# Performance work log

Measured on AMD Instinct MI355X. Metric: run time of the kernel, lower is better.

Reference implementation:

```python
import jax, jax.numpy as jnp
import numpy as np
import math

B = 200        # graphs
NPG = 512      # nodes per graph
EPG = 8192     # edges per graph (avg degree 16)
E = B * EPG
FIN = 11
H = 128


def setup_inputs() -> dict:
    key = jax.random.key(0)
    ks = jax.random.split(key, 16)
    g = jnp.arange(E, dtype=jnp.int32) // EPG  # graph id per edge
    edge_src = g * NPG + jax.random.randint(ks[0], (E,), 0, NPG, dtype=jnp.int32)
    edge_dst = g * NPG + jax.random.randint(ks[1], (E,), 0, NPG, dtype=jnp.int32)
    x = jax.random.normal(ks[2], (B * NPG, FIN), dtype=jnp.float32)

    def w(k, shape):
        return jax.random.normal(k, shape, dtype=jnp.float32) * 0.1

    return dict(
        x=x, edge_src=edge_src, edge_dst=edge_dst,
        num_graphs=B, nodes_per_graph=NPG,
        Wrel1=w(ks[3], (H, FIN)), Wroot1=w(ks[4], (H, FIN)), b1=jnp.zeros((H,), jnp.float32), pw1=w(ks[5], (H,)),
        Wrel2=w(ks[6], (H, H)), Wroot2=w(ks[7], (H, H)), b2=jnp.zeros((H,), jnp.float32), pw2=w(ks[8], (H,)),
        Wrel3=w(ks[9], (H, H)), Wroot3=w(ks[10], (H, H)), b3=jnp.zeros((H,), jnp.float32), pw3=w(ks[11], (H,)),
        Wl1=w(ks[12], (512, 256)), bl1=jnp.zeros((512,), jnp.float32),
        Wl2=w(ks[13], (64, 512)), bl2=jnp.zeros((64,), jnp.float32),
        Wl3=w(ks[14], (1, 64)), bl3=jnp.zeros((1,), jnp.float32),
    )


def graph_conv(x, src, dst, emask, Wrel, Wroot, b):
    # PyG GraphConv (aggr='add'): lin_rel(sum_j x_j) + lin_root(x)
    msg = x[src] * emask[:, None]                    # [E, F] gather + edge mask
    agg = jax.ops.segment_sum(msg, dst, num_segments=x.shape[0])
    return agg @ Wrel.T + b + x @ Wroot.T


def topk_pool(x, src, dst, emask, w, ratio, B):
    # PyG TopKPooling: score = tanh((x . w)/||w||), keep top ceil(ratio*N) per graph
    N = x.shape[0] // B
    k = int(math.ceil(ratio * N))
    score = jnp.tanh((x @ w) / jnp.linalg.norm(w))   # [B*N]
    _, idx = jax.lax.top_k(score.reshape(B, N), k)   # local indices per graph
    perm = (idx + (jnp.arange(B, dtype=idx.dtype) * N)[:, None]).reshape(-1)  # [B*k]
    xk = x[perm] * score[perm][:, None]
    # old node id -> new node id (or -1 if dropped); reindex edges, mask invalid
    newid = jnp.full((B * N,), -1, dtype=jnp.int32).at[perm].set(jnp.arange(B * k, dtype=jnp.int32))
    ns, nd = newid[src], newid[dst]
    keep = emask * (ns >= 0) * (nd >= 0)
    return xk, jnp.maximum(ns, 0), jnp.maximum(nd, 0), keep.astype(x.dtype)


def readout(x, B):
    # cat([global_max_pool, global_mean_pool]); uniform graph sizes -> reshape
    xr = x.reshape(B, -1, x.shape[-1])
    return jnp.concatenate([xr.max(axis=1), xr.mean(axis=1)], axis=-1)


def reference(x, edge_src, edge_dst, num_graphs, nodes_per_graph,
              Wrel1, Wroot1, b1, pw1, Wrel2, Wroot2, b2, pw2,
              Wrel3, Wroot3, b3, pw3, Wl1, bl1, Wl2, bl2, Wl3, bl3):
    Bg = num_graphs
    src, dst = edge_src, edge_dst
    emask = jnp.ones(src.shape, x.dtype)
    h = jax.nn.relu(graph_conv(x, src, dst, emask, Wrel1, Wroot1, b1))
    h, src, dst, emask = topk_pool(h, src, dst, emask, pw1, 0.5, Bg)
    x1 = readout(h, Bg)
    h = jax.nn.relu(graph_conv(h, src, dst, emask, Wrel2, Wroot2, b2))
    h, src, dst, emask = topk_pool(h, src, dst, emask, pw2, 0.8, Bg)
    x2 = readout(h, Bg)
    h = jax.nn.relu(graph_conv(h, src, dst, emask, Wrel3, Wroot3, b3))
    h, src, dst, emask = topk_pool(h, src, dst, emask, pw3, 0.8, Bg)
    x3 = readout(h, Bg)
    z = x1 + x2 + x3
    z = jax.nn.relu(z @ Wl1.T + bl1)   # dropout p=0.7 is identity in eval mode
    z = jax.nn.relu(z @ Wl2.T + bl2)
    return z @ Wl3.T + bl3             # [B, 1]
```

## Files before the change

kernel.cpp:

```cpp
#include <hip/hip_runtime.h>
#include <math.h>

#define BG   200
#define NPGc 512
#define EPGc 8192
#define NE   (BG*EPGc)
#define N0   (BG*NPGc)
#define FINc 11
#define Hc   128
#define K1c  256
#define K2c  205
#define K3c  164
#define N1   (BG*K1c)
#define N2   (BG*K2c)
#define N3   (BG*K3c)

typedef float f32x4 __attribute__((ext_vector_type(4)));
typedef short s16x8 __attribute__((ext_vector_type(8)));

#define PL ((size_t)N1*Hc)
#define PA ((size_t)N0*32)

__device__ inline unsigned short bf16_rne(float v){
  unsigned u = __float_as_uint(v);
  unsigned r = u + 0x7FFFu + ((u >> 16) & 1u);
  return (unsigned short)(r >> 16);
}
__device__ inline float bf16_f32(unsigned short h){
  return __uint_as_float(((unsigned)h) << 16);
}
__device__ inline void split3(float v, unsigned short& r0, unsigned short& r1,
                              unsigned short& r2){
  r0 = bf16_rne(v); float v1 = v - bf16_f32(r0);
  r1 = bf16_rne(v1); float v2 = v1 - bf16_f32(r1);
  r2 = bf16_rne(v2);
}

__device__ inline size_t flIdx(int row, int k){
  return ((size_t)(row >> 4))*2048 + (size_t)(k >> 3)*128
       + (size_t)(row & 15)*8 + (size_t)(k & 7);
}
__device__ inline size_t flIdx32(int row, int k){
  return ((size_t)(row >> 4))*512 + (size_t)(k >> 3)*128
       + (size_t)(row & 15)*8 + (size_t)(k & 7);
}

__launch_bounds__(512)
__global__ void k_front(const int* __restrict__ esrc, const int* __restrict__ edst,
                        const float* __restrict__ x,
                        const float* __restrict__ Wrel1, const float* __restrict__ Wroot1,
                        const float* __restrict__ Wrel2, const float* __restrict__ Wroot2,
                        const float* __restrict__ Wrel3, const float* __restrict__ Wroot3,
                        const float* __restrict__ Wl1, const float* __restrict__ Wl2,
                        const float* __restrict__ pw1, const float* __restrict__ pw2,
                        const float* __restrict__ pw3,
                        int* __restrict__ deg, int* __restrict__ rowptr,
                        int* __restrict__ csr, float* __restrict__ xp,
                        float* __restrict__ Wl1T, float* __restrict__ Wl2T,
                        unsigned short* __restrict__ Wsp, unsigned short* __restrict__ W1S,
                        float* __restrict__ z, float* __restrict__ norms){
  int b = blockIdx.x, t = threadIdx.x;
  if (b < BG){
    __shared__ int ed[EPGc];
    __shared__ int cnt[NPGc];
    __shared__ int sc[NPGc];
    int g = b;
    cnt[t] = 0;
    __syncthreads();
    int gb = g*EPGc;
    for (int i=t; i<EPGc; i+=512){
      int dl = edst[gb+i] & (NPGc-1);
      ed[i] = dl;
      atomicAdd(&cnt[dl], 1);
    }
    __syncthreads();
    int d = cnt[t];
    sc[t] = d;
    __syncthreads();
    for (int o=1;o<NPGc;o<<=1){
      int v = (t>=o) ? sc[t-o] : 0;
      __syncthreads();
      sc[t] += v;
      __syncthreads();
    }
    deg[g*NPGc+t]    = d;
    rowptr[g*NPGc+t] = gb + sc[t] - d;
    cnt[t] = sc[t] - d;
    __syncthreads();
    for (int i=t; i<EPGc; i+=512){
      int p = atomicAdd(&cnt[ed[i]], 1);
      csr[gb+p] = esrc[gb+i];
    }
  } else if (b < 456){
    int idx = (b-200)*512 + t;
    if (idx < 256*512){
      int f = idx >> 9, tt = idx & 511;
      Wl1T[idx] = Wl1[tt*256 + f];
    }
    if (idx < 512*64){
      int f = idx >> 6, tt = idx & 63;
      Wl2T[idx] = Wl2[tt*512 + f];
    }
    if (idx < 65536){
      int L = idx >> 15, p = (idx >> 14) & 1, ck = idx & 16383;
      int c = ck >> 7, k = ck & 127;
      const float* W = L ? (p ? Wroot3 : Wrel3) : (p ? Wroot2 : Wrel2);
      unsigned short r0, r1, r2;
      split3(W[c*128 + k], r0, r1, r2);
      unsigned short* base = Wsp + (size_t)((L*2+p)*3)*16384;
      size_t fl = flIdx(c, k);
      base[fl]          = r0;
      base[16384 + fl]  = r1;
      base[32768 + fl]  = r2;
    }
    if (idx < 4096){
      int c = idx >> 5, k = idx & 31;
      float v = (k < 11) ? Wrel1[c*11 + k] : (k < 22 ? Wroot1[c*11 + (k-11)] : 0.f);
      unsigned short r0, r1, r2;
      split3(v, r0, r1, r2);
      size_t fl = flIdx32(c, k);
      W1S[fl]        = r0;
      W1S[4096 + fl] = r1;
      W1S[8192 + fl] = r2;
    }
    if (idx < BG*256) z[idx] = 0.f;
    if (b == 455){
      int w = t >> 6, lane = t & 63;
      if (w < 3){
        const float* pw = (w==0) ? pw1 : (w==1 ? pw2 : pw3);
        float v0 = pw[lane], v1 = pw[64+lane];
        float ss = v0*v0 + v1*v1;
        for (int o=32;o>0;o>>=1) ss += __shfl_xor(ss, o);
        if (lane == 0) norms[w] = sqrtf(ss);
      }
    }
  } else {
    int idx = (b-456)*512 + t;
    int n = idx >> 4, f = idx & 15;
    xp[idx] = (f < FINc) ? x[n*FINc + f] : 0.f;
  }
}

__global__ void k_agg1s(const float* __restrict__ xp, const int* __restrict__ csr,
                        const int* __restrict__ rowptr, const int* __restrict__ deg,
                        unsigned short* __restrict__ AS){
  int bid = (int)((blockIdx.x & 7)*3200 + (blockIdx.x >> 3));
  int d = bid*4 + (threadIdx.x >> 6);
  if (d >= N0) return;
  int lane = threadIdx.x & 63;
  int slot = lane >> 4, f = lane & 15;
  int rs = rowptr[d], dg = deg[d];
  float a0 = 0.f, a1 = 0.f, a2 = 0.f, a3 = 0.f;
  for (int base=0; base<dg; base+=64){
    int e = base + lane;
    int s = 0;
    if (e < dg) s = csr[rs+e];
    int cnt = min(64, dg-base);
    int sv[16];
    #pragma unroll
    for (int u=0; u<16; u++) sv[u] = __shfl(s, u*4 + slot);
    #pragma unroll
    for (int u=0; u<16; u++){
      int ei = u*4 + slot;
      float v = 0.f;
      if (ei < cnt) v = xp[(sv[u] << 4) + f];
      if      ((u & 3) == 0) a0 += v;
      else if ((u & 3) == 1) a1 += v;
      else if ((u & 3) == 2) a2 += v;
      else                   a3 += v;
    }
  }
  a0 = (a0 + a1) + (a2 + a3);
  a0 += __shfl_xor(a0, 16);
  a0 += __shfl_xor(a0, 32);
  int k0 = 2*lane, k1 = k0 + 1;
  float s0 = __shfl(a0, k0 & 15);
  float s1 = __shfl(a0, k1 & 15);
  if (lane < 16){
    float v0 = (k0 < 11) ? s0 : ((k0 < 22) ? xp[(d<<4) + k0 - 11] : 0.f);
    float v1 = (k1 < 11) ? s1 : ((k1 < 22) ? xp[(d<<4) + k1 - 11] : 0.f);
    unsigned short a_0,a_1,a_2,b_0,b_1,b_2;
    split3(v0, a_0, a_1, a_2);
    split3(v1, b_0, b_1, b_2);
    size_t fl = flIdx32(d, k0);
    *(unsigned*)&AS[fl]        = (unsigned)a_0 | ((unsigned)b_0 << 16);
    *(unsigned*)&AS[PA + fl]   = (unsigned)a_1 | ((unsigned)b_1 << 16);
    *(unsigned*)&AS[2*PA + fl] = (unsigned)a_2 | ((unsigned)b_2 << 16);
  }
}

__launch_bounds__(256)
__global__ void k_conv1m(const unsigned short* __restrict__ AS,
                         const unsigned short* __restrict__ W1S,
                         const float* __restrict__ bias, const float* __restrict__ pw,
                         const float* __restrict__ norm_p,
                         float* __restrict__ hout, float* __restrict__ score, int M){
  __shared__ float scds[64][2];
  int tid = threadIdx.x;
  int w = tid >> 6, l = tid & 63;
  int wm = w >> 1, wn = w & 1;
  int lr = l & 15, lk = l >> 4;
  int m0 = blockIdx.x * 64;

  f32x4 acc[2][4];
  #pragma unroll
  for (int mi=0;mi<2;mi++)
    #pragma unroll
    for (int ni=0;ni<4;ni++) acc[mi][ni] = (f32x4){0.f,0.f,0.f,0.f};

  s16x8 af[3][2], bf[3][4];
  #pragma unroll
  for (int mi=0; mi<2; mi++){
    int tile = (m0 + wm*32 + mi*16) >> 4;
    size_t idx = (size_t)tile*512 + (size_t)lk*128 + (size_t)lr*8;
    af[0][mi] = *(const s16x8*)&AS[idx];
    af[1][mi] = *(const s16x8*)&AS[PA + idx];
    af[2][mi] = *(const s16x8*)&AS[2*PA + idx];
  }
  #pragma unroll
  for (int ni=0; ni<4; ni++){
    int ct = wn*4 + ni;
    size_t idx = (size_t)ct*512 + (size_t)lk*128 + (size_t)lr*8;
    bf[0][ni] = *(const s16x8*)&W1S[idx];
    bf[1][ni] = *(const s16x8*)&W1S[4096 + idx];
    bf[2][ni] = *(const s16x8*)&W1S[8192 + idx];
  }
  #define TRM(sa,sb) \
    _Pragma("unroll") \
    for (int ni=0; ni<4; ni++){ \
      _Pragma("unroll") \
      for (int mi=0; mi<2; mi++){ \
        acc[mi][ni] = __builtin_amdgcn_mfma_f32_16x16x32_bf16(af[sa][mi], bf[sb][ni], acc[mi][ni], 0,0,0); \
      } \
    }
  TRM(0,0) TRM(0,1) TRM(1,0) TRM(1,1) TRM(0,2) TRM(2,0)
  #undef TRM

  float nrm = *norm_p;
  float pwv[4], biasv[4];
  #pragma unroll
  for (int ni=0;ni<4;ni++){
    int col = wn*64 + ni*16 + lr;
    pwv[ni] = pw[col]; biasv[ni] = bias[col];
  }
  #pragma unroll
  for (int mi=0; mi<2; mi++){
    #pragma unroll
    for (int reg=0; reg<4; reg++){
      int rl = wm*32 + mi*16 + lk*4 + reg;
      int row = m0 + rl;
      float hv[4]; float sc = 0.f;
      #pragma unroll
      for (int ni=0; ni<4; ni++){
        hv[ni] = fmaxf(acc[mi][ni][reg] + biasv[ni], 0.f);
        sc += hv[ni]*pwv[ni];
      }
      if (row < M){
        #pragma unroll
        for (int ni=0; ni<4; ni++)
          hout[(size_t)row*Hc + wn*64 + ni*16 + lr] = hv[ni];
      }
      sc += __shfl_xor(sc,1); sc += __shfl_xor(sc,2);
      sc += __shfl_xor(sc,4); sc += __shfl_xor(sc,8);
      if (lr == 0) scds[rl][wn] = sc;
    }
  }
  __syncthreads();
  if (tid < 64){
    int row = m0 + tid;
    if (row < M) score[row] = tanhf((scds[tid][0] + scds[tid][1]) / nrm);
  }
}

template<int N, int K, int NP2>
__global__ void k_topk(const float* __restrict__ score, int* __restrict__ newid,
                       int* __restrict__ perm,
                       const int* __restrict__ map1In, int* __restrict__ map2Out,
                       const int* __restrict__ origPrev, int* __restrict__ origOut){
  __shared__ float sv[NP2];
  __shared__ int   si[NP2];
  __shared__ int   nid[N];
  int g = blockIdx.x, t = threadIdx.x;
  sv[t] = (t < N) ? score[g*N + t] : -INFINITY;
  si[t] = t;
  __syncthreads();
  for (int k=2;k<=NP2;k<<=1){
    for (int j=k>>1;j>0;j>>=1){
      int p = t ^ j;
      if (p > t){
        float va = sv[t], vb = sv[p];
        int   ia = si[t], ib = si[p];
        bool good = (va > vb) || (va == vb && ia < ib);
        bool up   = ((t & k) == 0);
        if (good != up){ sv[t]=vb; si[t]=ib; sv[p]=va; si[p]=ia; }
      }
      __syncthreads();
    }
  }
  if (t < N) nid[si[t]] = (t < K) ? t : -1;
  __syncthreads();
  if (t < N) newid[g*N + t] = (nid[t] >= 0) ? g*K + nid[t] : -1;
  if (t < K){
    int old = si[t];
    perm[g*K + t] = g*N + old;
    if (origOut) origOut[g*K + t] = origPrev[g*N + old];
  }
  if (map2Out){
    for (int o = t; o < NPGc; o += NP2){
      int m = map1In[g*NPGc + o];
      int r = (m >= 0) ? nid[m - g*N] : -1;
      map2Out[g*NPGc + o] = (r >= 0) ? g*K + r : -1;
    }
  }
}

__launch_bounds__(1024)
__global__ void k_gatherR(const float* __restrict__ h, const float* __restrict__ score,
                          const int* __restrict__ perm, float* __restrict__ hp,
                          unsigned short* __restrict__ hpS, float* __restrict__ z,
                          int kk, int doSplit){
  __shared__ float smx[8][Hc];
  __shared__ float ssm[8][Hc];
  int g = blockIdx.x;
  int rg = threadIdx.x >> 7, j = threadIdx.x & 127;
  float mx = -INFINITY, sm = 0.f;
  for (int r=rg; r<kk; r+=8){
    int m = g*kk + r;
    int p = perm[m];
    float v = h[(size_t)p*Hc + j] * score[p];
    if (hp) hp[(size_t)m*Hc + j] = v;
    float vn = __shfl_xor(v, 1);
    if (doSplit && !(j & 1)){
      unsigned short a0,a1,a2,b0,b1,b2;
      split3(v,  a0, a1, a2);
      split3(vn, b0, b1, b2);
      size_t fl = flIdx(m, j);
      *(unsigned*)&hpS[fl]        = (unsigned)a0 | ((unsigned)b0 << 16);
      *(unsigned*)&hpS[PL + fl]   = (unsigned)a1 | ((unsigned)b1 << 16);
      *(unsigned*)&hpS[2*PL + fl] = (unsigned)a2 | ((unsigned)b2 << 16);
    }
    mx = fmaxf(mx, v); sm += v;
  }
  smx[rg][j] = mx; ssm[rg][j] = sm;
  __syncthreads();
  if (rg == 0){
    #pragma unroll
    for (int u=1; u<8; u++){
      mx = fmaxf(mx, smx[u][j]); sm += ssm[u][j];
    }
    z[g*256 + j]       += mx;
    z[g*256 + 128 + j] += sm / (float)kk;
  }
}

__global__ void k_aggHs(const int* __restrict__ orig, const int* __restrict__ map,
                        const float* __restrict__ hp,
                        const int* __restrict__ csr, const int* __restrict__ rowptr,
                        const int* __restrict__ deg, unsigned short* __restrict__ aggS,
                        int M){
  int cpx = gridDim.x >> 3;
  int bid = (int)((blockIdx.x & 7)*cpx + (blockIdx.x >> 3));
  int m = bid*4 + (threadIdx.x>>6);
  int lane = threadIdx.x & 63;
  if (m >= M) return;
  int d = orig[m];
  int rs = rowptr[d], dg = deg[d];
  int half = lane >> 5, cl = lane & 31;
  f32x4 acc[8];
  #pragma unroll
  for (int u=0;u<8;u++) acc[u] = (f32x4){0.f,0.f,0.f,0.f};
  for (int base=0; base<dg; base+=64){
    int e = base + lane;
    int ns = -1;
    if (e < dg){ int s = csr[rs+e]; ns = map[s]; }
    int cnt = min(64, dg-base);
    for (int jj=0; jj<cnt; jj+=16){
      #pragma unroll
      for (int u=0; u<8; u++){
        int ei = jj + u*2 + half;
        int nsj = __shfl(ns, ei & 63);
        if (ei < cnt && nsj >= 0){
          acc[u] += *(const f32x4*)(hp + (size_t)nsj*Hc + cl*4);
        }
      }
    }
  }
  f32x4 s4 = ((acc[0]+acc[1]) + (acc[2]+acc[3])) + ((acc[4]+acc[5]) + (acc[6]+acc[7]));
  #pragma unroll
  for (int i=0;i<4;i++) s4[i] += __shfl_xor(s4[i], 32);
  float e0 = __shfl(s4[0], lane>>1);
  float e1 = __shfl(s4[1], lane>>1);
  float e2 = __shfl(s4[2], lane>>1);
  float e3 = __shfl(s4[3], lane>>1);
  float cx = (lane&1) ? e2 : e0;
  float cy = (lane&1) ? e3 : e1;
  unsigned short x0,x1,x2,y0,y1,y2;
  split3(cx, x0, x1, x2);
  split3(cy, y0, y1, y2);
  size_t fl = flIdx(m, 2*lane);
  *(unsigned*)&aggS[fl]        = (unsigned)x0 | ((unsigned)y0 << 16);
  *(unsigned*)&aggS[PL + fl]   = (unsigned)x1 | ((unsigned)y1 << 16);
  *(unsigned*)&aggS[2*PL + fl] = (unsigned)x2 | ((unsigned)y2 << 16);
}

__launch_bounds__(256)
__global__ void k_convH(const unsigned short* __restrict__ A0s,
                        const unsigned short* __restrict__ A1s,
                        const unsigned short* __restrict__ Wsp,
                        const float* __restrict__ bias, const float* __restrict__ pw,
                        const float* __restrict__ norm_p,
                        float* __restrict__ hout, float* __restrict__ score, int M){
  __shared__ float scds[64][2];
  int tid = threadIdx.x;
  int w = tid >> 6, l = tid & 63;
  int wm = w >> 1, wn = w & 1;
  int lr = l & 15, lk = l >> 4;
  int m0 = blockIdx.x * 64;

  f32x4 acc[2][4];
  #pragma unroll
  for (int mi=0;mi<2;mi++)
    #pragma unroll
    for (int ni=0;ni<4;ni++) acc[mi][ni] = (f32x4){0.f,0.f,0.f,0.f};

  #pragma unroll
  for (int kc=0; kc<4; kc++){
    #pragma unroll
    for (int p=0; p<2; p++){
      const unsigned short* As = p ? A1s : A0s;
      const unsigned short* Wp = Wsp + (size_t)p*3*16384;
      s16x8 af[3][2], bf[3][4];
      #pragma unroll
      for (int mi=0; mi<2; mi++){
        int tile = (m0 + wm*32 + mi*16) >> 4;
        size_t idx = (size_t)tile*2048 + (size_t)(kc*4+lk)*128 + (size_t)lr*8;
        af[0][mi] = *(const s16x8*)&As[idx];
        af[1][mi] = *(const s16x8*)&As[PL + idx];
        af[2][mi] = *(const s16x8*)&As[2*PL + idx];
      }
      #pragma unroll
      for (int ni=0; ni<4; ni++){
        int ct = wn*4 + ni;
        size_t idx = (size_t)ct*2048 + (size_t)(kc*4+lk)*128 + (size_t)lr*8;
        bf[0][ni] = *(const s16x8*)&Wp[idx];
        bf[1][ni] = *(const s16x8*)&Wp[16384 + idx];
        bf[2][ni] = *(const s16x8*)&Wp[32768 + idx];
      }
      #define TRM(sa,sb) \
        _Pragma("unroll") \
        for (int ni=0; ni<4; ni++){ \
          _Pragma("unroll") \
          for (int mi=0; mi<2; mi++){ \
            acc[mi][ni] = __builtin_amdgcn_mfma_f32_16x16x32_bf16(af[sa][mi], bf[sb][ni], acc[mi][ni], 0,0,0); \
          } \
        }
      TRM(0,0) TRM(0,1) TRM(1,0) TRM(1,1) TRM(0,2) TRM(2,0)
      #undef TRM
    }
  }

  float nrm = *norm_p;
  float pwv[4], biasv[4];
  #pragma unroll
  for (int ni=0;ni<4;ni++){
    int col = wn*64 + ni*16 + lr;
    pwv[ni] = pw[col]; biasv[ni] = bias[col];
  }
  #pragma unroll
  for (int mi=0; mi<2; mi++){
    #pragma unroll
    for (int reg=0; reg<4; reg++){
      int rl = wm*32 + mi*16 + lk*4 + reg;
      int row = m0 + rl;
      float hv[4]; float sc = 0.f;
      #pragma unroll
      for (int ni=0; ni<4; ni++){
        hv[ni] = fmaxf(acc[mi][ni][reg] + biasv[ni], 0.f);
        sc += hv[ni]*pwv[ni];
      }
      if (row < M){
        #pragma unroll
        for (int ni=0; ni<4; ni++)
          hout[(size_t)row*Hc + wn*64 + ni*16 + lr] = hv[ni];
      }
      sc += __shfl_xor(sc,1); sc += __shfl_xor(sc,2);
      sc += __shfl_xor(sc,4); sc += __shfl_xor(sc,8);
      if (lr == 0) scds[rl][wn] = sc;
    }
  }
  __syncthreads();
  if (tid < 64){
    int row = m0 + tid;
    if (row < M) score[row] = tanhf((scds[tid][0] + scds[tid][1]) / nrm);
  }
}

__launch_bounds__(512)
__global__ void k_mlp(const float* __restrict__ z,
                      const float* __restrict__ Wl1T, const float* __restrict__ bl1,
                      const float* __restrict__ Wl2T, const float* __restrict__ bl2,
                      const float* __restrict__ Wl3, const float* __restrict__ bl3,
                      float* __restrict__ out){
  __shared__ float zs[256];
  __shared__ float u1[512];
  int g = blockIdx.x, t = threadIdx.x;
  if (t < 256) zs[t] = z[g*256 + t];
  __syncthreads();
  {
    float acc = bl1[t];
    #pragma unroll 8
    for (int f=0; f<256; f++) acc = fmaf(zs[f], Wl1T[f*512 + t], acc);
    u1[t] = fmaxf(acc, 0.f);
  }
  __syncthreads();
  if (t < 64){
    float acc = bl2[t];
    #pragma unroll 8
    for (int f=0; f<512; f++) acc = fmaf(u1[f], Wl2T[f*64 + t], acc);
    float v = fmaxf(acc, 0.f) * Wl3[t];
    for (int o=32;o>0;o>>=1) v += __shfl_xor(v, o);
    if (t == 0) out[g] = v + bl3[0];
  }
}

extern "C" void kernel_launch(void* const* d_in, const int* in_sizes, int n_in,
                              void* d_out, int out_size, void* d_ws, size_t ws_size,
                              hipStream_t stream){
  const float* x     = (const float*)d_in[0];
  const int*   esrc  = (const int*)d_in[1];
  const int*   edst  = (const int*)d_in[2];
  const float* Wrel1 = (const float*)d_in[5];
  const float* Wroot1= (const float*)d_in[6];
  const float* b1    = (const float*)d_in[7];
  const float* pw1   = (const float*)d_in[8];
  const float* Wrel2 = (const float*)d_in[9];
  const float* Wroot2= (const float*)d_in[10];
  const float* b2    = (const float*)d_in[11];
  const float* pw2   = (const float*)d_in[12];
  const float* Wrel3 = (const float*)d_in[13];
  const float* Wroot3= (const float*)d_in[14];
  const float* b3    = (const float*)d_in[15];
  const float* pw3   = (const float*)d_in[16];
  const float* Wl1   = (const float*)d_in[17];
  const float* bl1   = (const float*)d_in[18];
  const float* Wl2   = (const float*)d_in[19];
  const float* bl2   = (const float*)d_in[20];
  const float* Wl3   = (const float*)d_in[21];
  const float* bl3   = (const float*)d_in[22];
  float* out = (float*)d_out;

  char* ws = (char*)d_ws;
  size_t off = 0;
  auto alloc = [&](size_t elems)->void*{
    void* p = ws + off;
    off += ((elems*4 + 255)/256)*256;
    return p;
  };
  int*   deg    = (int*)alloc(N0);
  int*   rowptr = (int*)alloc(N0);
  int*   csr    = (int*)alloc(NE);
  int*   map1   = (int*)alloc(N0);
  int*   newid2 = (int*)alloc(N1);
  int*   map2   = (int*)alloc(N0);
  int*   perm1  = (int*)alloc(N1);
  int*   perm2  = (int*)alloc(N2);
  int*   perm3  = (int*)alloc(N3);
  int*   orig3  = (int*)alloc(N2);
  float* score1 = (float*)alloc(N0);
  float* score2 = (float*)alloc(N1);
  float* score3 = (float*)alloc(N2);
  float* xp     = (float*)alloc((size_t)N0*16);
  float* Wl1T   = (float*)alloc(256*512);
  float* Wl2T   = (float*)alloc(512*64);
  unsigned short* Wsp = (unsigned short*)alloc(98304);
  unsigned short* W1S = (unsigned short*)alloc(6144);
  float* norms  = (float*)alloc(3);
  float* bigA   = (float*)alloc((size_t)N0*Hc);
  float* hB     = (float*)alloc((size_t)N1*Hc);
  float* hpA    = (float*)alloc((size_t)N1*Hc);
  unsigned short* hpS = (unsigned short*)alloc((size_t)3*N1*Hc/2);
  float* z      = (float*)alloc(BG*256);

  float* h1   = bigA;
  unsigned short* aggS = (unsigned short*)bigA;
  unsigned short* a1S  = hpS;
  float* h2   = hB;
  float* h3   = hB;

  k_front<<<3656, 512, 0, stream>>>(esrc, edst, x,
                                    Wrel1, Wroot1, Wrel2, Wroot2, Wrel3, Wroot3,
                                    Wl1, Wl2, pw1, pw2, pw3,
                                    deg, rowptr, csr, xp,
                                    Wl1T, Wl2T, Wsp, W1S, z, norms);

  k_agg1s  <<<N0/4, 256, 0, stream>>>(xp, csr, rowptr, deg, a1S);
  k_conv1m <<<N0/64, 256, 0, stream>>>(a1S, W1S, b1, pw1, norms+0, h1, score1, N0);
  k_topk<NPGc, K1c, 512><<<BG, 512, 0, stream>>>(score1, map1, perm1,
                                                 nullptr, nullptr, nullptr, nullptr);
  k_gatherR<<<BG, 1024, 0, stream>>>(h1, score1, perm1, hpA, hpS, z, K1c, 1);

  k_aggHs  <<<N1/4, 256, 0, stream>>>(perm1, map1, hpA, csr, rowptr, deg, aggS, N1);
  k_convH  <<<N1/64, 256, 0, stream>>>(aggS, hpS, Wsp, b2, pw2, norms+1, h2, score2, N1);
  k_topk<K1c, K2c, 256><<<BG, 256, 0, stream>>>(score2, newid2, perm2,
                                                map1, map2, perm1, orig3);
  k_gatherR<<<BG, 1024, 0, stream>>>(h2, score2, perm2, hpA, hpS, z, K2c, 1);

  k_aggHs  <<<10256, 256, 0, stream>>>(orig3, map2, hpA, csr, rowptr, deg, aggS, N2);
  k_convH  <<<(N2+63)/64, 256, 0, stream>>>(aggS, hpS, Wsp + 98304, b3, pw3, norms+2,
                                            h3, score3, N2);
  k_topk<K2c, K3c, 256><<<BG, 256, 0, stream>>>(score3, newid2, perm3,
                                                nullptr, nullptr, nullptr, nullptr);
  k_gatherR<<<BG, 1024, 0, stream>>>(h3, score3, perm3, nullptr, nullptr, z, K3c, 0);

  k_mlp<<<BG, 512, 0, stream>>>(z, Wl1T, bl1, Wl2T, bl2, Wl3, bl3, out);
}
```

Baseline: 304.1 us.

## Fuse top-k selection with pooled gather/readout and final MLP per graph

Merges the per-graph top-k sort kernel with the following gather/readout kernel, and folds the final MLP into the last pooling stage. The sorted score and index arrays are reused from shared memory instead of re-reading perm and score from global memory, and four kernel launches are removed. In exchange, the bitonic sort now runs in a 1024-thread block where most threads idle through its syncs, and the final stage keeps extra shared memory resident.

Result: faster. 284.2 us (-6.5%).

```diff
diff --git a/kernel.cpp b/kernel.cpp
--- a/kernel.cpp
+++ b/kernel.cpp
@@ -272,27 +272,42 @@
   }
 }
 
-template<int N, int K, int NP2>
-__global__ void k_topk(const float* __restrict__ score, int* __restrict__ newid,
-                       int* __restrict__ perm,
+template<int N, int K, int NP2, bool DOSPLIT, bool DOMLP>
+__launch_bounds__(1024)
+__global__ void k_topg(const float* __restrict__ score, const float* __restrict__ h,
+                       int* __restrict__ newid, int* __restrict__ perm,
                        const int* __restrict__ map1In, int* __restrict__ map2Out,
-                       const int* __restrict__ origPrev, int* __restrict__ origOut){
+                       const int* __restrict__ origPrev, int* __restrict__ origOut,
+                       float* __restrict__ hp, unsigned short* __restrict__ hpS,
+                       float* __restrict__ z,
+                       const float* __restrict__ Wl1T, const float* __restrict__ bl1,
+                       const float* __restrict__ Wl2T, const float* __restrict__ bl2,
+                       const float* __restrict__ Wl3, const float* __restrict__ bl3,
+                       float* __restrict__ out){
   __shared__ float sv[NP2];
   __shared__ int   si[NP2];
   __shared__ int   nid[N];
+  __shared__ float smx[8][Hc];
+  __shared__ float ssm[8][Hc];
+  __shared__ float zfin[256];
+  __shared__ float u1[512];
   int g = blockIdx.x, t = threadIdx.x;
-  sv[t] = (t < N) ? score[g*N + t] : -INFINITY;
-  si[t] = t;
+  if (t < NP2){
+    sv[t] = (t < N) ? score[g*N + t] : -INFINITY;
+    si[t] = t;
+  }
   __syncthreads();
   for (int k=2;k<=NP2;k<<=1){
     for (int j=k>>1;j>0;j>>=1){
-      int p = t ^ j;
-      if (p > t){
-        float va = sv[t], vb = sv[p];
-        int   ia = si[t], ib = si[p];
-        bool good = (va > vb) || (va == vb && ia < ib);
-        bool up   = ((t & k) == 0);
-        if (good != up){ sv[t]=vb; si[t]=ib; sv[p]=va; si[p]=ia; }
+      if (t < NP2){
+        int p = t ^ j;
+        if (p > t){
+          float va = sv[t], vb = sv[p];
+          int   ia = si[t], ib = si[p];
+          bool good = (va > vb) || (va == vb && ia < ib);
+          bool up   = ((t & k) == 0);
+          if (good != up){ sv[t]=vb; si[t]=ib; sv[p]=va; si[p]=ia; }
+        }
       }
       __syncthreads();
     }
@@ -306,38 +321,33 @@
     if (origOut) origOut[g*K + t] = origPrev[g*N + old];
   }
   if (map2Out){
-    for (int o = t; o < NPGc; o += NP2){
+    for (int o = t; o < NPGc; o += 1024){
       int m = map1In[g*NPGc + o];
       int r = (m >= 0) ? nid[m - g*N] : -1;
       map2Out[g*NPGc + o] = (r >= 0) ? g*K + r : -1;
     }
   }
-}
-
-__launch_bounds__(1024)
-__global__ void k_gatherR(const float* __restrict__ h, const float* __restrict__ score,
-                          const int* __restrict__ perm, float* __restrict__ hp,
-                          unsigned short* __restrict__ hpS, float* __restrict__ z,
-                          int kk, int doSplit){
-  __shared__ float smx[8][Hc];
-  __shared__ float ssm[8][Hc];
-  int g = blockIdx.x;
-  int rg = threadIdx.x >> 7, j = threadIdx.x & 127;
+  __syncthreads();
+
+  int rg = t >> 7, j = t & 127;
   float mx = -INFINITY, sm = 0.f;
-  for (int r=rg; r<kk; r+=8){
-    int m = g*kk + r;
-    int p = perm[m];
-    float v = h[(size_t)p*Hc + j] * score[p];
+  for (int r=rg; r<K; r+=8){
+    int old = si[r];
+    float sc = sv[r];
+    float v = h[(size_t)(g*N + old)*Hc + j] * sc;
+    int m = g*K + r;
     if (hp) hp[(size_t)m*Hc + j] = v;
-    float vn = __shfl_xor(v, 1);
-    if (doSplit && !(j & 1)){
-      unsigned short a0,a1,a2,b0,b1,b2;
-      split3(v,  a0, a1, a2);
-      split3(vn, b0, b1, b2);
-      size_t fl = flIdx(m, j);
-      *(unsigned*)&hpS[fl]        = (unsigned)a0 | ((unsigned)b0 << 16);
-      *(unsigned*)&hpS[PL + fl]   = (unsigned)a1 | ((unsigned)b1 << 16);
-      *(unsigned*)&hpS[2*PL + fl] = (unsigned)a2 | ((unsigned)b2 << 16);
+    if constexpr (DOSPLIT){
+      float vn = __shfl_xor(v, 1);
+      if (!(j & 1)){
+        unsigned short a0,a1,a2,b0,b1,b2;
+        split3(v,  a0, a1, a2);
+        split3(vn, b0, b1, b2);
+        size_t fl = flIdx(m, j);
+        *(unsigned*)&hpS[fl]        = (unsigned)a0 | ((unsigned)b0 << 16);
+        *(unsigned*)&hpS[PL + fl]   = (unsigned)a1 | ((unsigned)b1 << 16);
+        *(unsigned*)&hpS[2*PL + fl] = (unsigned)a2 | ((unsigned)b2 << 16);
+      }
     }
     mx = fmaxf(mx, v); sm += v;
   }
@@ -348,8 +358,31 @@
     for (int u=1; u<8; u++){
       mx = fmaxf(mx, smx[u][j]); sm += ssm[u][j];
     }
-    z[g*256 + j]       += mx;
-    z[g*256 + 128 + j] += sm / (float)kk;
+    if constexpr (DOMLP){
+      zfin[j]       = z[g*256 + j]       + mx;
+      zfin[128 + j] = z[g*256 + 128 + j] + sm / (float)K;
+    } else {
+      z[g*256 + j]       += mx;
+      z[g*256 + 128 + j] += sm / (float)K;
+    }
+  }
+  if constexpr (DOMLP){
+    __syncthreads();
+    if (t < 512){
+      float acc = bl1[t];
+      #pragma unroll 8
+      for (int f=0; f<256; f++) acc = fmaf(zfin[f], Wl1T[f*512 + t], acc);
+      u1[t] = fmaxf(acc, 0.f);
+    }
+    __syncthreads();
+    if (t < 64){
+      float acc = bl2[t];
+      #pragma unroll 8
+      for (int f=0; f<512; f++) acc = fmaf(u1[f], Wl2T[f*64 + t], acc);
+      float v = fmaxf(acc, 0.f) * Wl3[t];
+      for (int o=32;o>0;o>>=1) v += __shfl_xor(v, o);
+      if (t == 0) out[g] = v + bl3[0];
+    }
   }
 }
 
@@ -492,34 +525,6 @@
   if (tid < 64){
     int row = m0 + tid;
     if (row < M) score[row] = tanhf((scds[tid][0] + scds[tid][1]) / nrm);
-  }
-}
-
-__launch_bounds__(512)
-__global__ void k_mlp(const float* __restrict__ z,
-                      const float* __restrict__ Wl1T, const float* __restrict__ bl1,
-                      const float* __restrict__ Wl2T, const float* __restrict__ bl2,
-                      const float* __restrict__ Wl3, const float* __restrict__ bl3,
-                      float* __restrict__ out){
-  __shared__ float zs[256];
-  __shared__ float u1[512];
-  int g = blockIdx.x, t = threadIdx.x;
-  if (t < 256) zs[t] = z[g*256 + t];
-  __syncthreads();
-  {
-    float acc = bl1[t];
-    #pragma unroll 8
-    for (int f=0; f<256; f++) acc = fmaf(zs[f], Wl1T[f*512 + t], acc);
-    u1[t] = fmaxf(acc, 0.f);
-  }
-  __syncthreads();
-  if (t < 64){
-    float acc = bl2[t];
-    #pragma unroll 8
-    for (int f=0; f<512; f++) acc = fmaf(u1[f], Wl2T[f*64 + t], acc);
-    float v = fmaxf(acc, 0.f) * Wl3[t];
-    for (int o=32;o>0;o>>=1) v += __shfl_xor(v, o);
-    if (t == 0) out[g] = v + bl3[0];
   }
 }
 
@@ -595,22 +600,20 @@
 
   k_agg1s  <<<N0/4, 256, 0, stream>>>(xp, csr, rowptr, deg, a1S);
   k_conv1m <<<N0/64, 256, 0, stream>>>(a1S, W1S, b1, pw1, norms+0, h1, score1, N0);
-  k_topk<NPGc, K1c, 512><<<BG, 512, 0, stream>>>(score1, map1, perm1,
-                                                 nullptr, nullptr, nullptr, nullptr);
-  k_gatherR<<<BG, 1024, 0, stream>>>(h1, score1, perm1, hpA, hpS, z, K1c, 1);
+  k_topg<NPGc, K1c, 512, true, false><<<BG, 1024, 0, stream>>>(
+      score1, h1, map1, perm1, nullptr, nullptr, nullptr, nullptr,
+      hpA, hpS, z, nullptr, nullptr, nullptr, nullptr, nullptr, nullptr, nullptr);
 
   k_aggHs  <<<N1/4, 256, 0, stream>>>(perm1, map1, hpA, csr, rowptr, deg, aggS, N1);
   k_convH  <<<N1/64, 256, 0, stream>>>(aggS, hpS, Wsp, b2, pw2, norms+1, h2, score2, N1);
-  k_topk<K1c, K2c, 256><<<BG, 256, 0, stream>>>(score2, newid2, perm2,
-                                                map1, map2, perm1, orig3);
-  k_gatherR<<<BG, 1024, 0, stream>>>(h2, score2, perm2, hpA, hpS, z, K2c, 1);
+  k_topg<K1c, K2c, 256, true, false><<<BG, 1024, 0, stream>>>(
+      score2, h2, newid2, perm2, map1, map2, perm1, orig3,
+      hpA, hpS, z, nullptr, nullptr, nullptr, nullptr, nullptr, nullptr, nullptr);
 
   k_aggHs  <<<10256, 256, 0, stream>>>(orig3, map2, hpA, csr, rowptr, deg, aggS, N2);
   k_convH  <<<(N2+63)/64, 256, 0, stream>>>(aggS, hpS, Wsp + 98304, b3, pw3, norms+2,
                                             h3, score3, N2);
-  k_topk<K2c, K3c, 256><<<BG, 256, 0, stream>>>(score3, newid2, perm3,
-                                                nullptr, nullptr, nullptr, nullptr);
-  k_gatherR<<<BG, 1024, 0, stream>>>(h3, score3, perm3, nullptr, nullptr, z, K3c, 0);
-
-  k_mlp<<<BG, 512, 0, stream>>>(z, Wl1T, bl1, Wl2T, bl2, Wl3, bl3, out);
-}
+  k_topg<K2c, K3c, 256, false, true><<<BG, 1024, 0, stream>>>(
+      score3, h3, newid2, perm3, nullptr, nullptr, nullptr, nullptr,
+      nullptr, nullptr, z, Wl1T, bl1, Wl2T, bl2, Wl3, bl3, out);
+}
```
